# Optimization experiments

Hardware: AMD Instinct MI355X
Metric: run time of the kernel (lower is better)

## Reference

```python
import jax, jax.numpy as jnp
import numpy as np

#   per angular channel l: out_l = (1/sqrt(2l+1)) * sum_m x_nu[n,m,q] * x_1[n,m,p]
#   stacked over l with zero padding in the m axis (pad beyond 2l+1 is zero,
#   so the m-sum is unaffected), features flattened as full (q, p) outer product.

L = 4       # l = 0..3
N = 50000   # atomic environments (samples)
M = 7       # 2*l_max + 1
F_NU = 32   # features of density_nu per l
F_1 = 16    # features of density_1 per l


def setup_inputs() -> dict:
    key = jax.random.key(0)
    k1, k2 = jax.random.split(key)
    x_nu = jax.random.normal(k1, (L, N, M, F_NU), dtype=jnp.float32)
    x_1 = jax.random.normal(k2, (L, N, M, F_1), dtype=jnp.float32)
    ls = jnp.arange(L)
    # mask m-components beyond 2l+1 for each l  -> [L, M]
    mmask = (jnp.arange(M)[None, :] < (2 * ls + 1)[:, None]).astype(jnp.float32)
    x_nu = x_nu * mmask[:, None, :, None]
    x_1 = x_1 * mmask[:, None, :, None]
    return {"x_nu": x_nu, "x_1": x_1}


def reference(x_nu, x_1):
    # x_nu: [L, N, M, F_nu], x_1: [L, N, M, F_1]
    l_dim, n, _, f_nu = x_nu.shape
    f_1 = x_1.shape[-1]
    cg = 1.0 / jnp.sqrt(2.0 * jnp.arange(l_dim, dtype=jnp.float32) + 1.0)  # [L]
    # full (q_nu, q_1) outer product with sum over m, per l
    out = jnp.einsum('lnmq,lnmp->nlqp', x_nu, x_1)  # [N, L, F_nu, F_1]
    out = out * cg[None, :, None, None]
    return out.reshape(n, l_dim * f_nu * f_1)  # [N, L*F_nu*F_1]
```

## Files before the change

kernel.cpp:

```cpp
#include <hip/hip_runtime.h>


constexpr int L_DIM  = 4;
constexpr int M_DIM  = 7;
constexpr int FNU    = 32;
constexpr int F1     = 16;
constexpr int XNU_W  = L_DIM * M_DIM * FNU;
constexpr int X1_W   = L_DIM * M_DIM * F1;
constexpr int SAMP_W = XNU_W + X1_W;
constexpr int OUT_W  = L_DIM * FNU * F1;

__global__ __launch_bounds__(256) void ps_kernel(
    const float* __restrict__ x_nu,
    const float* __restrict__ x_1,
    float* __restrict__ out,
    int N)
{
    __shared__ float lds[2 * SAMP_W];
    const int t  = threadIdx.x;
    const int n0 = blockIdx.x * 2;

    const float4* __restrict__ xnu4 = reinterpret_cast<const float4*>(x_nu);
    const float4* __restrict__ x14  = reinterpret_cast<const float4*>(x_1);
    float4* lds4 = reinterpret_cast<float4*>(lds);

    #pragma unroll
    for (int ii = 0; ii < 3; ++ii) {
        int i = t + ii * 256;
        if (i < 2 * 336) {
            int s = (i >= 336) ? 1 : 0;
            int r = i - s * 336;
            int n = n0 + s;
            if (n < N) {
                float4 v; int dst;
                if (r < 224) {
                    int l = r / 56, off = r - l * 56;
                    v   = xnu4[(size_t)(l * N + n) * 56 + off];
                    dst = s * (SAMP_W / 4) + l * 56 + off;
                } else {
                    int r2 = r - 224;
                    int l = r2 / 28, off = r2 - l * 28;
                    v   = x14[(size_t)(l * N + n) * 28 + off];
                    dst = s * (SAMP_W / 4) + (XNU_W / 4) + l * 28 + off;
                }
                lds4[dst] = v;
            }
        }
    }
    __syncthreads();

    const int s  = t >> 7;
    const int u7 = t & 127;
    const int l  = u7 >> 5;
    const int u  = u7 & 31;
    const int pb = (u & 3) * 4;
    const int q2 = u >> 2;

    const int n = n0 + s;
    if (n >= N) return;

    const float* xnu_s = lds + s * SAMP_W + l * (M_DIM * FNU);
    const float* x1_s  = lds + s * SAMP_W + XNU_W + l * (M_DIM * F1);

    float acc[4][4];
    #pragma unroll
    for (int k = 0; k < 4; ++k)
        #pragma unroll
        for (int j = 0; j < 4; ++j) acc[k][j] = 0.0f;

    #pragma unroll
    for (int m = 0; m < M_DIM; ++m) {
        float4 b = *reinterpret_cast<const float4*>(&x1_s[m * F1 + pb]);
        float a[4];
        #pragma unroll
        for (int k = 0; k < 4; ++k) a[k] = xnu_s[m * FNU + q2 + 8 * k];
        #pragma unroll
        for (int k = 0; k < 4; ++k) {
            acc[k][0] += a[k] * b.x;
            acc[k][1] += a[k] * b.y;
            acc[k][2] += a[k] * b.z;
            acc[k][3] += a[k] * b.w;
        }
    }

    const float scale = rsqrtf(2.0f * (float)l + 1.0f);
    float* outp = out + (size_t)n * OUT_W + l * (FNU * F1);
    #pragma unroll
    for (int k = 0; k < 4; ++k) {
        int q = q2 + 8 * k;
        float4 v = make_float4(acc[k][0] * scale, acc[k][1] * scale,
                               acc[k][2] * scale, acc[k][3] * scale);
        *reinterpret_cast<float4*>(&outp[q * F1 + pb]) = v;
    }
}

extern "C" void kernel_launch(void* const* d_in, const int* in_sizes, int n_in,
                              void* d_out, int out_size, void* d_ws, size_t ws_size,
                              hipStream_t stream) {
    const float* x_nu = (const float*)d_in[0];
    const float* x_1  = (const float*)d_in[1];
    float* out = (float*)d_out;
    const int N = in_sizes[0] / XNU_W;
    const int blocks = (N + 1) / 2;
    ps_kernel<<<blocks, 256, 0, stream>>>(x_nu, x_1, out, N);
}
```

Before: 567.4 us.

## Process four samples per block with contiguous loads and nontemporal output stores

Each block now handles four consecutive samples instead of two. Loads for each l become contiguous runs, with a fast path that skips the per-element index division, and each thread computes two samples. Output is written with nontemporal stores so the large write stream bypasses the cache. This halves the block count and increases LDS use per block, which may reduce occupancy.

```diff
diff --git a/kernel.cpp b/kernel.cpp
--- a/kernel.cpp
+++ b/kernel.cpp
@@ -1,14 +1,17 @@
 #include <hip/hip_runtime.h>
 
 
-constexpr int L_DIM  = 4;
-constexpr int M_DIM  = 7;
-constexpr int FNU    = 32;
-constexpr int F1     = 16;
-constexpr int XNU_W  = L_DIM * M_DIM * FNU;
-constexpr int X1_W   = L_DIM * M_DIM * F1;
-constexpr int SAMP_W = XNU_W + X1_W;
-constexpr int OUT_W  = L_DIM * FNU * F1;
+typedef float v4f __attribute__((ext_vector_type(4)));
+
+constexpr int L_DIM = 4, M_DIM = 7, FNU = 32, F1 = 16;
+constexpr int XNU_S = M_DIM * FNU;
+constexpr int X1_S  = M_DIM * F1;
+constexpr int NS    = 4;
+constexpr int A_LL  = NS * XNU_S;
+constexpr int BOFF  = L_DIM * A_LL;
+constexpr int B_LL  = NS * X1_S + 16;
+constexpr int LDS_F = BOFF + L_DIM * B_LL;
+constexpr int OUT_W = L_DIM * FNU * F1;
 
 __global__ __launch_bounds__(256) void ps_kernel(
     const float* __restrict__ x_nu,
@@ -16,81 +19,90 @@
     float* __restrict__ out,
     int N)
 {
-    __shared__ float lds[2 * SAMP_W];
+    __shared__ float lds[LDS_F];
     const int t  = threadIdx.x;
-    const int n0 = blockIdx.x * 2;
+    const int n0 = blockIdx.x * NS;
 
     const float4* __restrict__ xnu4 = reinterpret_cast<const float4*>(x_nu);
     const float4* __restrict__ x14  = reinterpret_cast<const float4*>(x_1);
     float4* lds4 = reinterpret_cast<float4*>(lds);
 
-    #pragma unroll
-    for (int ii = 0; ii < 3; ++ii) {
-        int i = t + ii * 256;
-        if (i < 2 * 336) {
-            int s = (i >= 336) ? 1 : 0;
-            int r = i - s * 336;
-            int n = n0 + s;
-            if (n < N) {
-                float4 v; int dst;
-                if (r < 224) {
-                    int l = r / 56, off = r - l * 56;
-                    v   = xnu4[(size_t)(l * N + n) * 56 + off];
-                    dst = s * (SAMP_W / 4) + l * 56 + off;
-                } else {
-                    int r2 = r - 224;
-                    int l = r2 / 28, off = r2 - l * 28;
-                    v   = x14[(size_t)(l * N + n) * 28 + off];
-                    dst = s * (SAMP_W / 4) + (XNU_W / 4) + l * 28 + off;
-                }
-                lds4[dst] = v;
+    if (n0 + NS <= N) {
+        #pragma unroll
+        for (int l = 0; l < L_DIM; ++l) {
+            const float4* src_a = xnu4 + (size_t)(l * N + n0) * (XNU_S / 4);
+            const float4* src_b = x14  + (size_t)(l * N + n0) * (X1_S / 4);
+            float4* dst_a = lds4 + l * (A_LL / 4);
+            float4* dst_b = lds4 + (BOFF / 4) + l * (B_LL / 4);
+            if (t < 224) dst_a[t] = src_a[t];
+            else         dst_b[t - 224] = src_b[t - 224];
+            int i2 = t + 32;
+            if (t < 80) dst_b[i2] = src_b[i2];
+        }
+    } else {
+        for (int i = t; i < L_DIM * NS * (XNU_S + X1_S) / 4; i += 256) {
+            int l = i / 336, r = i - l * 336;
+            if (r < 224) {
+                int s = r / 56, off = r - s * 56;
+                if (n0 + s < N)
+                    lds4[l * (A_LL / 4) + s * 56 + off] =
+                        xnu4[(size_t)(l * N + n0 + s) * 56 + off];
+            } else {
+                int r2 = r - 224;
+                int s = r2 / 28, off = r2 - s * 28;
+                if (n0 + s < N)
+                    lds4[(BOFF / 4) + l * (B_LL / 4) + s * 28 + off] =
+                        x14[(size_t)(l * N + n0 + s) * 28 + off];
             }
         }
     }
     __syncthreads();
 
-    const int s  = t >> 7;
-    const int u7 = t & 127;
-    const int l  = u7 >> 5;
-    const int u  = u7 & 31;
-    const int pb = (u & 3) * 4;
-    const int q2 = u >> 2;
-
-    const int n = n0 + s;
-    if (n >= N) return;
-
-    const float* xnu_s = lds + s * SAMP_W + l * (M_DIM * FNU);
-    const float* x1_s  = lds + s * SAMP_W + XNU_W + l * (M_DIM * F1);
-
-    float acc[4][4];
-    #pragma unroll
-    for (int k = 0; k < 4; ++k)
-        #pragma unroll
-        for (int j = 0; j < 4; ++j) acc[k][j] = 0.0f;
+    const int l     = (t >> 5) & 3;
+    const int u     = t & 31;
+    const int pb    = (u & 3) * 4;
+    const int q2    = u >> 2;
+    const int sbase = t >> 7;
+    const float scale = rsqrtf(2.0f * (float)l + 1.0f);
 
     #pragma unroll
-    for (int m = 0; m < M_DIM; ++m) {
-        float4 b = *reinterpret_cast<const float4*>(&x1_s[m * F1 + pb]);
-        float a[4];
+    for (int si = 0; si < 2; ++si) {
+        const int s = sbase + 2 * si;
+        const int n = n0 + s;
+        if (n >= N) continue;
+
+        const float* a_s = lds + l * A_LL + s * XNU_S;
+        const float* b_s = lds + BOFF + l * B_LL + s * X1_S;
+
+        float acc[4][4];
         #pragma unroll
-        for (int k = 0; k < 4; ++k) a[k] = xnu_s[m * FNU + q2 + 8 * k];
+        for (int k = 0; k < 4; ++k)
+            #pragma unroll
+            for (int j = 0; j < 4; ++j) acc[k][j] = 0.0f;
+
+        #pragma unroll
+        for (int m = 0; m < M_DIM; ++m) {
+            v4f b = *reinterpret_cast<const v4f*>(&b_s[m * F1 + pb]);
+            float a[4];
+            #pragma unroll
+            for (int k = 0; k < 4; ++k) a[k] = a_s[m * FNU + q2 + 8 * k];
+            #pragma unroll
+            for (int k = 0; k < 4; ++k) {
+                acc[k][0] += a[k] * b.x;
+                acc[k][1] += a[k] * b.y;
+                acc[k][2] += a[k] * b.z;
+                acc[k][3] += a[k] * b.w;
+            }
+        }
+
+        float* outp = out + (size_t)n * OUT_W + l * (FNU * F1);
         #pragma unroll
         for (int k = 0; k < 4; ++k) {
-            acc[k][0] += a[k] * b.x;
-            acc[k][1] += a[k] * b.y;
-            acc[k][2] += a[k] * b.z;
-            acc[k][3] += a[k] * b.w;
+            v4f v = { acc[k][0] * scale, acc[k][1] * scale,
+                      acc[k][2] * scale, acc[k][3] * scale };
+            __builtin_nontemporal_store(
+                v, reinterpret_cast<v4f*>(&outp[(q2 + 8 * k) * F1 + pb]));
         }
-    }
-
-    const float scale = rsqrtf(2.0f * (float)l + 1.0f);
-    float* outp = out + (size_t)n * OUT_W + l * (FNU * F1);
-    #pragma unroll
-    for (int k = 0; k < 4; ++k) {
-        int q = q2 + 8 * k;
-        float4 v = make_float4(acc[k][0] * scale, acc[k][1] * scale,
-                               acc[k][2] * scale, acc[k][3] * scale);
-        *reinterpret_cast<float4*>(&outp[q * F1 + pb]) = v;
     }
 }
 
@@ -100,7 +112,7 @@
     const float* x_nu = (const float*)d_in[0];
     const float* x_1  = (const float*)d_in[1];
     float* out = (float*)d_out;
-    const int N = in_sizes[0] / XNU_W;
-    const int blocks = (N + 1) / 2;
+    const int N = in_sizes[0] / (L_DIM * M_DIM * FNU);
+    const int blocks = (N + NS - 1) / NS;
     ps_kernel<<<blocks, 256, 0, stream>>>(x_nu, x_1, out, N);
 }
```

Measured after the change: 584.7 us. +3.0%, slower.
